# Kernel optimization log

Hardware: AMD Instinct MI355X
Metric: run time of the kernel (lower is better)

The kernel has to match this reference:

```python
import jax, jax.numpy as jnp
import numpy as np

EPS = 1e-6  # config.model.train_hparams.eps
DIM_MODEL = 512
DIM_K = 64  # dim_q = dim_k = dim_v


def setup_inputs() -> dict:
    key = jax.random.key(0)
    ks = jax.random.split(key, 10)
    B, S = 8, 2048
    query = jax.random.normal(ks[0], (B, S, DIM_MODEL), dtype=jnp.float32)
    key_t = jax.random.normal(ks[1], (B, S, DIM_MODEL), dtype=jnp.float32)
    value = jax.random.normal(ks[2], (B, S, DIM_MODEL), dtype=jnp.float32)
    attention_mask = jax.random.randint(ks[3], (B, S, S), 0, 2, dtype=jnp.int32)
    lim = 1.0 / np.sqrt(DIM_MODEL)
    Wq = jax.random.uniform(ks[4], (DIM_K, DIM_MODEL), jnp.float32, -lim, lim)
    bq = jax.random.uniform(ks[5], (DIM_K,), jnp.float32, -lim, lim)
    Wk = jax.random.uniform(ks[6], (DIM_K, DIM_MODEL), jnp.float32, -lim, lim)
    bk = jax.random.uniform(ks[7], (DIM_K,), jnp.float32, -lim, lim)
    Wv = jax.random.uniform(ks[8], (DIM_K, DIM_MODEL), jnp.float32, -lim, lim)
    bv = jax.random.uniform(ks[9], (DIM_K,), jnp.float32, -lim, lim)
    return {"query": query, "key": key_t, "value": value,
            "attention_mask": attention_mask,
            "Wq": Wq, "bq": bq, "Wk": Wk, "bk": bk, "Wv": Wv, "bv": bv}


def reference(query, key, value, attention_mask, Wq, bq, Wk, bk, Wv, bv):
    scale = DIM_K ** (-0.5)
    q = jnp.einsum('bsm,dm->bsd', query, Wq) + bq   # (B,S,dk)
    k = jnp.einsum('bsm,dm->bsd', key, Wk) + bk
    v = jnp.einsum('bsm,dm->bsd', value, Wv) + bv
    qk = jnp.einsum('bqd,bkd->bqk', q, k) * scale   # (B,S,S)
    qk = jnp.where(qk == 0, EPS, qk)                 # masked_fill(qk == 0, eps)
    qk = jnp.where(attention_mask == 0, EPS, qk)     # masked_fill(mask == 0, eps)
    attention_weight = jax.nn.softmax(qk, axis=-1)
    attention = jnp.einsum('bqk,bkd->bqd', attention_weight, v)
    return attention, attention_weight
```

## Files before the change

kernel.cpp:

```cpp
#include <hip/hip_runtime.h>

#define BATCH 8
#define SEQ   2048
#define DM    512
#define DK    64
#define NROW  (BATCH*SEQ)
#define EPSV  1e-6f

typedef _Float16 f16x8 __attribute__((ext_vector_type(8)));
typedef _Float16 f16x4 __attribute__((ext_vector_type(4)));
typedef float    f32x4 __attribute__((ext_vector_type(4)));

#define MFMA16(a,b,c) __builtin_amdgcn_mfma_f32_16x16x32_f16(a, b, c, 0, 0, 0)

__global__ void wcvt(const float* __restrict__ wq, const float* __restrict__ wk,
                     const float* __restrict__ wv, _Float16* __restrict__ w16) {
    int idx = (blockIdx.x * 256 + threadIdx.x) * 4;
    int z = idx >> 15;
    int off = idx & 32767;
    const float* src = (z == 0) ? wq : ((z == 1) ? wk : wv);
    float4 g = *reinterpret_cast<const float4*>(src + off);
    f16x4 h = { (_Float16)g.x, (_Float16)g.y, (_Float16)g.z, (_Float16)g.w };
    *reinterpret_cast<f16x4*>(w16 + idx) = h;
}

__global__ __launch_bounds__(256) void proj(
    const float* __restrict__ query, const float* __restrict__ key,
    const float* __restrict__ value, const _Float16* __restrict__ w16,
    const float* __restrict__ bq, const float* __restrict__ bk, const float* __restrict__ bv,
    _Float16* __restrict__ q16, _Float16* __restrict__ k16, _Float16* __restrict__ vT16)
{
    __shared__ _Float16 xsh[64][72];

    const int t = threadIdx.x;
    const int wave = t >> 6, lane = t & 63;
    const int n16 = lane & 15, quad = lane >> 4;
    const int z = blockIdx.y;
    const float* in   = (z == 0) ? query : ((z == 1) ? key : value);
    const float* bias = (z == 0) ? bq    : ((z == 1) ? bk  : bv);
    const _Float16* wz = w16 + z * (DK * DM);
    const int row0 = blockIdx.x * 64;
    const float* abase = in + (size_t)(row0 + wave * 16 + n16) * DM + quad * 8;

    f32x4 acc[4] = {};

    float4 p0 = *reinterpret_cast<const float4*>(abase);
    float4 p1 = *reinterpret_cast<const float4*>(abase + 4);
    float4 p2 = *reinterpret_cast<const float4*>(abase + 32);
    float4 p3 = *reinterpret_cast<const float4*>(abase + 36);

    #pragma unroll 2
    for (int kk = 0; kk < DM; kk += 64) {
        f16x8 a0 = { (_Float16)p0.x, (_Float16)p0.y, (_Float16)p0.z, (_Float16)p0.w,
                     (_Float16)p1.x, (_Float16)p1.y, (_Float16)p1.z, (_Float16)p1.w };
        f16x8 a1 = { (_Float16)p2.x, (_Float16)p2.y, (_Float16)p2.z, (_Float16)p2.w,
                     (_Float16)p3.x, (_Float16)p3.y, (_Float16)p3.z, (_Float16)p3.w };
        if (kk < DM - 64) {
            p0 = *reinterpret_cast<const float4*>(abase + kk + 64);
            p1 = *reinterpret_cast<const float4*>(abase + kk + 68);
            p2 = *reinterpret_cast<const float4*>(abase + kk + 96);
            p3 = *reinterpret_cast<const float4*>(abase + kk + 100);
        }
        #pragma unroll
        for (int nt = 0; nt < 4; ++nt) {
            const _Float16* bbase = wz + (size_t)(nt * 16 + n16) * DM + kk + quad * 8;
            f16x8 b0 = *reinterpret_cast<const f16x8*>(bbase);
            f16x8 b1 = *reinterpret_cast<const f16x8*>(bbase + 32);
            acc[nt] = MFMA16(a0, b0, acc[nt]);
            acc[nt] = MFMA16(a1, b1, acc[nt]);
        }
    }

    const int batch = row0 >> 11, row0s = row0 & (SEQ - 1);
    if (z < 2) {
        _Float16* out = (z == 0) ? q16 : k16;
        #pragma unroll
        for (int nt = 0; nt < 4; ++nt) {
            float bzv = bias[nt * 16 + n16];
            #pragma unroll
            for (int r = 0; r < 4; ++r) {
                int grow = row0 + wave * 16 + quad * 4 + r;
                out[(size_t)grow * DK + nt * 16 + n16] = (_Float16)(acc[nt][r] + bzv);
            }
        }
    } else {
        #pragma unroll
        for (int nt = 0; nt < 4; ++nt) {
            float bzv = bias[nt * 16 + n16];
            #pragma unroll
            for (int r = 0; r < 4; ++r)
                xsh[nt * 16 + n16][wave * 16 + quad * 4 + r] = (_Float16)(acc[nt][r] + bzv);
        }
        __syncthreads();
        int d = t >> 2, s0 = (t & 3) * 16;
        _Float16* dst = vT16 + ((size_t)(batch * DK + d)) * SEQ + row0s + s0;
        f16x8 h0, h1;
        #pragma unroll
        for (int j = 0; j < 8; ++j) { h0[j] = xsh[d][s0 + j]; h1[j] = xsh[d][s0 + 8 + j]; }
        *reinterpret_cast<f16x8*>(dst)     = h0;
        *reinterpret_cast<f16x8*>(dst + 8) = h1;
    }
}

#define RT  16
#define SCH 2056

__global__ __launch_bounds__(512, 4) void attn(
    const _Float16* __restrict__ q16,
    const _Float16* __restrict__ k16,
    const _Float16* __restrict__ vT16,
    const int* __restrict__ mask,
    float* __restrict__ attno,
    float* __restrict__ aw)
{
    __shared__ _Float16 sc[RT][SCH];
    __shared__ float red[4][16][17];
    __shared__ float st_il[RT];

    const int t = threadIdx.x;
    const int wave = t >> 6, lane = t & 63;
    const int n16 = lane & 15, quad = lane >> 4;
    const int row0 = blockIdx.x * RT;
    const int batch = row0 >> 11, row0s = row0 & (SEQ - 1);

    {
        const _Float16* qb = q16 + (size_t)(row0 + n16) * DK + quad * 8;
        f16x8 aq0 = *reinterpret_cast<const f16x8*>(qb);
        f16x8 aq1 = *reinterpret_cast<const f16x8*>(qb + 32);
        const _Float16* kbase = k16 + (size_t)(batch * SEQ) * DK;
        const _Float16* kb = kbase + (size_t)(wave * 16 + n16) * DK + quad * 8;
        f16x8 b0 = *reinterpret_cast<const f16x8*>(kb);
        f16x8 b1 = *reinterpret_cast<const f16x8*>(kb + 32);
        for (int c = 0; c < 16; ++c) {
            f16x8 cb0 = b0, cb1 = b1;
            if (c < 15) {
                const _Float16* nb = kbase + (size_t)((c + 1) * 128 + wave * 16 + n16) * DK + quad * 8;
                b0 = *reinterpret_cast<const f16x8*>(nb);
                b1 = *reinterpret_cast<const f16x8*>(nb + 32);
            }
            f32x4 acc = {};
            acc = MFMA16(aq0, cb0, acc);
            acc = MFMA16(aq1, cb1, acc);
            int col = c * 128 + wave * 16 + n16;
            #pragma unroll
            for (int r = 0; r < 4; ++r)
                sc[quad * 4 + r][col] = (_Float16)(acc[r] * 0.125f);
        }
    }
    __syncthreads();

    #pragma unroll 1
    for (int rr = 0; rr < 2; ++rr) {
        int row = wave * 2 + rr;
        const int4* mrow = reinterpret_cast<const int4*>(
            mask + (size_t)batch * SEQ * SEQ + (size_t)(row0s + row) * SEQ);

        float vmax = -3.4e38f;
        #pragma unroll
        for (int it = 0; it < 8; ++it) {
            int j = it * 64 + lane;
            int4  m4 = mrow[j];
            f16x4 s4 = *reinterpret_cast<const f16x4*>(&sc[row][j * 4]);
            float s0 = (float)s4[0], s1 = (float)s4[1], s2 = (float)s4[2], s3 = (float)s4[3];
            s0 = (m4.x == 0 || s0 == 0.0f) ? EPSV : s0;
            s1 = (m4.y == 0 || s1 == 0.0f) ? EPSV : s1;
            s2 = (m4.z == 0 || s2 == 0.0f) ? EPSV : s2;
            s3 = (m4.w == 0 || s3 == 0.0f) ? EPSV : s3;
            f16x4 h = { (_Float16)s0, (_Float16)s1, (_Float16)s2, (_Float16)s3 };
            *reinterpret_cast<f16x4*>(&sc[row][j * 4]) = h;
            vmax = fmaxf(vmax, fmaxf(fmaxf(s0, s1), fmaxf(s2, s3)));
        }
        #pragma unroll
        for (int off = 32; off; off >>= 1) vmax = fmaxf(vmax, __shfl_xor(vmax, off));

        float vsum = 0.0f;
        #pragma unroll
        for (int it = 0; it < 8; ++it) {
            int j = it * 64 + lane;
            f16x4 s4 = *reinterpret_cast<const f16x4*>(&sc[row][j * 4]);
            float e0 = __expf((float)s4[0] - vmax), e1 = __expf((float)s4[1] - vmax);
            float e2 = __expf((float)s4[2] - vmax), e3 = __expf((float)s4[3] - vmax);
            f16x4 h = { (_Float16)e0, (_Float16)e1, (_Float16)e2, (_Float16)e3 };
            *reinterpret_cast<f16x4*>(&sc[row][j * 4]) = h;
            vsum += (e0 + e1) + (e2 + e3);
        }
        #pragma unroll
        for (int off = 32; off; off >>= 1) vsum += __shfl_xor(vsum, off);
        float il = 1.0f / vsum;
        if (lane == 0) st_il[row] = il;

        float* awrow = aw + (size_t)batch * SEQ * SEQ + (size_t)(row0s + row) * SEQ;
        #pragma unroll
        for (int it = 0; it < 8; ++it) {
            int j = it * 64 + lane;
            f16x4 e4 = *reinterpret_cast<const f16x4*>(&sc[row][j * 4]);
            float4 p4 = { (float)e4[0] * il, (float)e4[1] * il,
                          (float)e4[2] * il, (float)e4[3] * il };
            *reinterpret_cast<float4*>(awrow + j * 4) = p4;
        }
    }
    __syncthreads();

    {
        const int dblk = wave & 3, khalf = wave >> 2;
        f32x4 oacc = {};
        const _Float16* vbase = vT16 + ((size_t)(batch * DK + dblk * 16 + n16)) * SEQ
                              + khalf * 1024;
        const _Float16* scrow = &sc[n16][khalf * 1024];
        f16x8 bv0 = *reinterpret_cast<const f16x8*>(vbase + quad * 8);
        f16x8 bv1 = *reinterpret_cast<const f16x8*>(vbase + 32 + quad * 8);
        for (int c = 0; c < 16; ++c) {
            f16x8 cb0 = bv0, cb1 = bv1;
            if (c < 15) {
                bv0 = *reinterpret_cast<const f16x8*>(vbase + (c + 1) * 64 + quad * 8);
                bv1 = *reinterpret_cast<const f16x8*>(vbase + (c + 1) * 64 + 32 + quad * 8);
            }
            f16x8 a0 = *reinterpret_cast<const f16x8*>(scrow + c * 64 + quad * 8);
            f16x8 a1 = *reinterpret_cast<const f16x8*>(scrow + c * 64 + 32 + quad * 8);
            oacc = MFMA16(a0, cb0, oacc);
            oacc = MFMA16(a1, cb1, oacc);
        }
        if (khalf == 1) {
            #pragma unroll
            for (int r = 0; r < 4; ++r)
                red[dblk][quad * 4 + r][n16] = oacc[r];
        }
        __syncthreads();
        if (khalf == 0) {
            #pragma unroll
            for (int r = 0; r < 4; ++r) {
                int row = quad * 4 + r;
                float o = oacc[r] + red[dblk][row][n16];
                attno[(size_t)(row0 + row) * DK + dblk * 16 + n16] = o * st_il[row];
            }
        }
    }
}

extern "C" void kernel_launch(void* const* d_in, const int* in_sizes, int n_in,
                              void* d_out, int out_size, void* d_ws, size_t ws_size,
                              hipStream_t stream) {
    const float* query = (const float*)d_in[0];
    const float* key   = (const float*)d_in[1];
    const float* value = (const float*)d_in[2];
    const int*   amask = (const int*)d_in[3];
    const float* Wq = (const float*)d_in[4];
    const float* bq = (const float*)d_in[5];
    const float* Wk = (const float*)d_in[6];
    const float* bk = (const float*)d_in[7];
    const float* Wv = (const float*)d_in[8];
    const float* bv = (const float*)d_in[9];

    float* attno = (float*)d_out;
    float* aw    = attno + (size_t)NROW * DK;

    char* ws = (char*)d_ws;
    _Float16* q16  = (_Float16*)(ws);
    _Float16* k16  = (_Float16*)(ws + (size_t)2097152);
    _Float16* vT16 = (_Float16*)(ws + (size_t)4194304);
    _Float16* w16  = (_Float16*)(ws + (size_t)6291456);

    wcvt<<<96, 256, 0, stream>>>(Wq, Wk, Wv, w16);
    proj<<<dim3(NROW / 64, 3), 256, 0, stream>>>(query, key, value, w16,
                                                 bq, bk, bv, q16, k16, vT16);
    attn<<<NROW / RT, 512, 0, stream>>>(q16, k16, vT16, amask, attno, aw);
}
```

Before: 369.5 us.

## Prefetch mask into bitmasks before QK, deepen K/V prefetch, nontemporal weight stores

Loads each wave's two mask rows at kernel start and packs them into per-lane 32-bit bitmasks, so mask traffic overlaps the QK^T MFMA phase instead of stalling the softmax loop. K and V tile prefetch goes from one iteration ahead to two, with the loops fully unrolled. Attention-weight output is written with nontemporal stores to reduce cache pollution. This raises register pressure under launch_bounds(512,4), which may cause spills or lower occupancy.

```diff
diff --git a/kernel.cpp b/kernel.cpp
--- a/kernel.cpp
+++ b/kernel.cpp
@@ -123,20 +123,44 @@
     const int row0 = blockIdx.x * RT;
     const int batch = row0 >> 11, row0s = row0 & (SEQ - 1);
 
+    unsigned int mb0 = 0, mb1 = 0;
+    {
+        const int4* mr0 = reinterpret_cast<const int4*>(
+            mask + (size_t)batch * SEQ * SEQ + (size_t)(row0s + wave * 2) * SEQ);
+        const int4* mr1 = mr0 + SEQ / 4;
+        #pragma unroll
+        for (int it = 0; it < 8; ++it) {
+            int4 a = mr0[it * 64 + lane];
+            int4 b = mr1[it * 64 + lane];
+            mb0 |= ((a.x != 0) ? 1u : 0u) << (it * 4 + 0);
+            mb0 |= ((a.y != 0) ? 1u : 0u) << (it * 4 + 1);
+            mb0 |= ((a.z != 0) ? 1u : 0u) << (it * 4 + 2);
+            mb0 |= ((a.w != 0) ? 1u : 0u) << (it * 4 + 3);
+            mb1 |= ((b.x != 0) ? 1u : 0u) << (it * 4 + 0);
+            mb1 |= ((b.y != 0) ? 1u : 0u) << (it * 4 + 1);
+            mb1 |= ((b.z != 0) ? 1u : 0u) << (it * 4 + 2);
+            mb1 |= ((b.w != 0) ? 1u : 0u) << (it * 4 + 3);
+        }
+    }
+
     {
         const _Float16* qb = q16 + (size_t)(row0 + n16) * DK + quad * 8;
         f16x8 aq0 = *reinterpret_cast<const f16x8*>(qb);
         f16x8 aq1 = *reinterpret_cast<const f16x8*>(qb + 32);
-        const _Float16* kbase = k16 + (size_t)(batch * SEQ) * DK;
-        const _Float16* kb = kbase + (size_t)(wave * 16 + n16) * DK + quad * 8;
-        f16x8 b0 = *reinterpret_cast<const f16x8*>(kb);
-        f16x8 b1 = *reinterpret_cast<const f16x8*>(kb + 32);
+        const _Float16* kbase = k16 + (size_t)(batch * SEQ) * DK
+                              + (size_t)(wave * 16 + n16) * DK + quad * 8;
+        f16x8 b0[2], b1[2];
+        b0[0] = *reinterpret_cast<const f16x8*>(kbase);
+        b1[0] = *reinterpret_cast<const f16x8*>(kbase + 32);
+        b0[1] = *reinterpret_cast<const f16x8*>(kbase + 128 * DK);
+        b1[1] = *reinterpret_cast<const f16x8*>(kbase + 128 * DK + 32);
+        #pragma unroll
         for (int c = 0; c < 16; ++c) {
-            f16x8 cb0 = b0, cb1 = b1;
-            if (c < 15) {
-                const _Float16* nb = kbase + (size_t)((c + 1) * 128 + wave * 16 + n16) * DK + quad * 8;
-                b0 = *reinterpret_cast<const f16x8*>(nb);
-                b1 = *reinterpret_cast<const f16x8*>(nb + 32);
+            int cur = c & 1;
+            f16x8 cb0 = b0[cur], cb1 = b1[cur];
+            if (c < 14) {
+                b0[cur] = *reinterpret_cast<const f16x8*>(kbase + (size_t)(c + 2) * 128 * DK);
+                b1[cur] = *reinterpret_cast<const f16x8*>(kbase + (size_t)(c + 2) * 128 * DK + 32);
             }
             f32x4 acc = {};
             acc = MFMA16(aq0, cb0, acc);
@@ -152,20 +176,18 @@
     #pragma unroll 1
     for (int rr = 0; rr < 2; ++rr) {
         int row = wave * 2 + rr;
-        const int4* mrow = reinterpret_cast<const int4*>(
-            mask + (size_t)batch * SEQ * SEQ + (size_t)(row0s + row) * SEQ);
+        unsigned int mb = rr ? mb1 : mb0;
 
         float vmax = -3.4e38f;
         #pragma unroll
         for (int it = 0; it < 8; ++it) {
             int j = it * 64 + lane;
-            int4  m4 = mrow[j];
             f16x4 s4 = *reinterpret_cast<const f16x4*>(&sc[row][j * 4]);
             float s0 = (float)s4[0], s1 = (float)s4[1], s2 = (float)s4[2], s3 = (float)s4[3];
-            s0 = (m4.x == 0 || s0 == 0.0f) ? EPSV : s0;
-            s1 = (m4.y == 0 || s1 == 0.0f) ? EPSV : s1;
-            s2 = (m4.z == 0 || s2 == 0.0f) ? EPSV : s2;
-            s3 = (m4.w == 0 || s3 == 0.0f) ? EPSV : s3;
+            s0 = (!((mb >> (it * 4 + 0)) & 1u) || s0 == 0.0f) ? EPSV : s0;
+            s1 = (!((mb >> (it * 4 + 1)) & 1u) || s1 == 0.0f) ? EPSV : s1;
+            s2 = (!((mb >> (it * 4 + 2)) & 1u) || s2 == 0.0f) ? EPSV : s2;
+            s3 = (!((mb >> (it * 4 + 3)) & 1u) || s3 == 0.0f) ? EPSV : s3;
             f16x4 h = { (_Float16)s0, (_Float16)s1, (_Float16)s2, (_Float16)s3 };
             *reinterpret_cast<f16x4*>(&sc[row][j * 4]) = h;
             vmax = fmaxf(vmax, fmaxf(fmaxf(s0, s1), fmaxf(s2, s3)));
@@ -194,9 +216,9 @@
         for (int it = 0; it < 8; ++it) {
             int j = it * 64 + lane;
             f16x4 e4 = *reinterpret_cast<const f16x4*>(&sc[row][j * 4]);
-            float4 p4 = { (float)e4[0] * il, (float)e4[1] * il,
-                          (float)e4[2] * il, (float)e4[3] * il };
-            *reinterpret_cast<float4*>(awrow + j * 4) = p4;
+            f32x4 p4 = { (float)e4[0] * il, (float)e4[1] * il,
+                         (float)e4[2] * il, (float)e4[3] * il };
+            __builtin_nontemporal_store(p4, reinterpret_cast<f32x4*>(awrow + j * 4));
         }
     }
     __syncthreads();
@@ -205,15 +227,20 @@
         const int dblk = wave & 3, khalf = wave >> 2;
         f32x4 oacc = {};
         const _Float16* vbase = vT16 + ((size_t)(batch * DK + dblk * 16 + n16)) * SEQ
-                              + khalf * 1024;
+                              + khalf * 1024 + quad * 8;
         const _Float16* scrow = &sc[n16][khalf * 1024];
-        f16x8 bv0 = *reinterpret_cast<const f16x8*>(vbase + quad * 8);
-        f16x8 bv1 = *reinterpret_cast<const f16x8*>(vbase + 32 + quad * 8);
+        f16x8 bv0[2], bv1[2];
+        bv0[0] = *reinterpret_cast<const f16x8*>(vbase);
+        bv1[0] = *reinterpret_cast<const f16x8*>(vbase + 32);
+        bv0[1] = *reinterpret_cast<const f16x8*>(vbase + 64);
+        bv1[1] = *reinterpret_cast<const f16x8*>(vbase + 96);
+        #pragma unroll
         for (int c = 0; c < 16; ++c) {
-            f16x8 cb0 = bv0, cb1 = bv1;
-            if (c < 15) {
-                bv0 = *reinterpret_cast<const f16x8*>(vbase + (c + 1) * 64 + quad * 8);
-                bv1 = *reinterpret_cast<const f16x8*>(vbase + (c + 1) * 64 + 32 + quad * 8);
+            int cur = c & 1;
+            f16x8 cb0 = bv0[cur], cb1 = bv1[cur];
+            if (c < 14) {
+                bv0[cur] = *reinterpret_cast<const f16x8*>(vbase + (c + 2) * 64);
+                bv1[cur] = *reinterpret_cast<const f16x8*>(vbase + (c + 2) * 64 + 32);
             }
             f16x8 a0 = *reinterpret_cast<const f16x8*>(scrow + c * 64 + quad * 8);
             f16x8 a1 = *reinterpret_cast<const f16x8*>(scrow + c * 64 + 32 + quad * 8);
```

Result: no change. 368.7 us (-0.2%).
